# Optimization experiments

Measured on AMD Instinct MI355X. Metric: run time of the kernel, lower is better.

Reference implementation:

```python
import jax, jax.numpy as jnp
import numpy as np


def setup_inputs() -> dict:
    key = jax.random.key(0)
    ks = jax.random.split(key, 6)
    B, S, D = 2, 2048, 1024
    E, DFF = 8, 2048  # E includes always-on expert 0; router sees E-1 routed experts
    scale = 0.02
    return {
        "hidden_states": jax.random.normal(ks[0], (B, S, D), dtype=jnp.float32),
        "router_w": jax.random.normal(ks[1], (D, E - 1), dtype=jnp.float32) * scale,
        "router_b": jnp.zeros((E - 1,), dtype=jnp.float32),
        "wg": jax.random.normal(ks[2], (E, D, DFF), dtype=jnp.float32) * scale,
        "wu": jax.random.normal(ks[3], (E, D, DFF), dtype=jnp.float32) * scale,
        "wd": jax.random.normal(ks[4], (E, DFF, D), dtype=jnp.float32) * scale,
        "top_k": 2,
    }


def _expert_mlp(x, wg_e, wu_e, wd_e):
    # SwiGLU MLP: down( silu(x @ gate) * (x @ up) )
    return (jax.nn.silu(x @ wg_e) * (x @ wu_e)) @ wd_e


def reference(hidden_states, router_w, router_b, wg, wu, wd, top_k):
    B, S, D = hidden_states.shape
    E = wg.shape[0]  # total experts incl. always-on expert 0
    x = hidden_states.reshape(-1, D)  # [T, D]
    T = x.shape[0]

    # Router over E-1 routed experts, softmax in float32
    router_logits = x @ router_w + router_b  # [T, E-1]
    probs = jax.nn.softmax(router_logits.astype(jnp.float32), axis=-1)
    topw, topi = jax.lax.top_k(probs, top_k)  # [T, k]
    topw = topw / jnp.sum(topw, axis=-1, keepdims=True)
    topw = topw.astype(x.dtype)

    # Dense combine weights over routed experts (0 for unselected)
    cw = jnp.zeros((T, E - 1), dtype=x.dtype)
    cw = cw.at[jnp.arange(T)[:, None], topi].add(topw)  # [T, E-1]

    # Always-on expert 0 with weight 1
    out = _expert_mlp(x, wg[0], wu[0], wd[0])  # [T, D]

    # Routed experts 1..E-1 (static small loop over experts)
    for e in range(1, E):
        ye = _expert_mlp(x, wg[e], wu[e], wd[e])  # [T, D]
        out = out + cw[:, e - 1, None] * ye

    return out.reshape(B, S, -1)
```

## Files before the change

### kernel.cpp

```cpp
#include <hip/hip_runtime.h>

#define T_TOK 4096
#define DIM   1024
#define DFF   2048
#define NE    8
#define NR    7
#define MAXNB 71
#define NY    (32 + MAXNB)

typedef __bf16 bf16x8 __attribute__((ext_vector_type(8)));
typedef float  floatx4 __attribute__((ext_vector_type(4)));

__device__ __forceinline__ unsigned short f32_bf16(float f) {
  union { float f; unsigned int u; } v; v.f = f;
  unsigned int u = v.u;
  unsigned int r = (u + 0x7FFFu + ((u >> 16) & 1u)) >> 16;
  return (unsigned short)r;
}

typedef __attribute__((address_space(3))) void lds_void_t;
typedef const __attribute__((address_space(1))) void g_void_t;

__device__ __forceinline__ void gld16(const void* g, void* l) {
  __builtin_amdgcn_global_load_lds((g_void_t*)g, (lds_void_t*)l, 16, 0, 0);
}

__global__ __launch_bounds__(256) void cvt_x_kernel(const float4* __restrict__ in,
                                                    ushort4* __restrict__ out) {
  int i = blockIdx.x * 256 + threadIdx.x;
  float4 v = in[i];
  ushort4 o;
  o.x = f32_bf16(v.x); o.y = f32_bf16(v.y);
  o.z = f32_bf16(v.z); o.w = f32_bf16(v.w);
  out[i] = o;
}

__global__ __launch_bounds__(256) void router_kernel(const float* __restrict__ x,
                                                     const float* __restrict__ rw,
                                                     const float* __restrict__ rb,
                                                     int* __restrict__ idxR,
                                                     float* __restrict__ wslR,
                                                     int* __restrict__ cnt,
                                                     int4* __restrict__ tokE,
                                                     float2* __restrict__ tokW) {
  const int lane = threadIdx.x & 63;
  const int t = blockIdx.x * 4 + (threadIdx.x >> 6);
  const float* xr = x + (size_t)t * DIM;
  float acc[NR];
#pragma unroll
  for (int e = 0; e < NR; e++) acc[e] = 0.f;
  for (int d = lane; d < DIM; d += 64) {
    float xv = xr[d];
#pragma unroll
    for (int e = 0; e < NR; e++) acc[e] += xv * rw[d * NR + e];
  }
#pragma unroll
  for (int off = 32; off > 0; off >>= 1) {
#pragma unroll
    for (int e = 0; e < NR; e++) acc[e] += __shfl_xor(acc[e], off, 64);
  }
  if (lane == 0) {
    float lg[NR];
    float m = -1e30f;
#pragma unroll
    for (int e = 0; e < NR; e++) { lg[e] = acc[e] + rb[e]; m = fmaxf(m, lg[e]); }
    float p[NR], s = 0.f;
#pragma unroll
    for (int e = 0; e < NR; e++) { p[e] = expf(lg[e] - m); s += p[e]; }
#pragma unroll
    for (int e = 0; e < NR; e++) p[e] /= s;
    int i1 = 0;
#pragma unroll
    for (int e = 1; e < NR; e++) if (p[e] > p[i1]) i1 = e;
    int i2 = (i1 == 0) ? 1 : 0;
#pragma unroll
    for (int e = 0; e < NR; e++) if (e != i1 && p[e] > p[i2]) i2 = e;
    float w1 = p[i1], w2 = p[i2], sw = w1 + w2;
    float w1n = w1 / sw, w2n = w2 / sw;
    int s1 = atomicAdd(&cnt[i1], 1);
    idxR[i1 * 4096 + s1] = t; wslR[i1 * 4096 + s1] = w1n;
    int s2 = atomicAdd(&cnt[i2], 1);
    idxR[i2 * 4096 + s2] = t; wslR[i2 * 4096 + s2] = w2n;
    int4 te; te.x = i1; te.y = s1; te.z = i2; te.w = s2;
    tokE[t] = te;
    float2 tw; tw.x = w1n; tw.y = w2n;
    tokW[t] = tw;
  }
}

__global__ __launch_bounds__(256) void sched_kernel(const int* __restrict__ cnt,
                                                    int* __restrict__ idxR,
                                                    float* __restrict__ wslR,
                                                    int4* __restrict__ schedAll,
                                                    int4* __restrict__ schedP,
                                                    int* __restrict__ prefOut,
                                                    int rsb) {
  __shared__ int nb[NR], pref[NR];
  if (threadIdx.x == 0) {
    int p = 0;
    for (int e = 0; e < NR; e++) { int c = cnt[e]; int n = (c + 127) >> 7; nb[e] = n; pref[e] = p; p += n; }
  }
  __syncthreads();
  if (threadIdx.x < NR) prefOut[threadIdx.x] = pref[threadIdx.x];
  for (int e = 0; e < NR; e++) {
    int c = cnt[e], top = nb[e] * 128;
    for (int i = c + (int)threadIdx.x; i < top; i += 256) {
      idxR[e * 4096 + i] = 0; wslR[e * 4096 + i] = 0.f;
    }
  }
  const int NBtot = pref[NR - 1] + nb[NR - 1];
  for (int y = threadIdx.x; y < 32; y += 256) {
    int4 ent; ent.x = 0; ent.y = -1; ent.z = y * 128; ent.w = 0;
    schedAll[y] = ent;
  }
  for (int y = threadIdx.x; y < MAXNB; y += 256) {
    int4 ent; ent.x = -1; ent.y = 0; ent.z = 0; ent.w = 0;
    if (y < NBtot) {
#pragma unroll
      for (int e = 0; e < NR; e++)
        if (y >= pref[e] && y < pref[e] + nb[e]) {
          int rb2 = y - pref[e];
          ent.x = e + 1; ent.y = e * 4096 + rb2 * 128; ent.z = rsb + y * 128;
        }
    }
    schedAll[32 + y] = ent;
  }
  for (int i = threadIdx.x; i < NR * 32; i += 256) {
    int e = i >> 5, rb2 = i & 31;
    int4 ent; ent.w = 0;
    if (rb2 < nb[e]) { ent.x = e + 1; ent.y = e * 4096 + rb2 * 128; ent.z = rb2 * 128; }
    else             { ent.x = -1; ent.y = 0; ent.z = 0; }
    schedP[i] = ent;
  }
}

__global__ __launch_bounds__(256) void transpose_cvt_kernel(
    const float* __restrict__ wg, const float* __restrict__ wu, const float* __restrict__ wd,
    unsigned short* __restrict__ wgt, unsigned short* __restrict__ wut,
    unsigned short* __restrict__ wdt) {
  __shared__ float tile[64][33];
  const int z = blockIdx.z;
  const float* src; unsigned short* dst; int R, C;
  if (z < 8)       { src = wg + (size_t)z * DIM * DFF;        dst = wgt + (size_t)z * DIM * DFF;        R = DIM; C = DFF; }
  else if (z < 16) { src = wu + (size_t)(z - 8) * DIM * DFF;  dst = wut + (size_t)(z - 8) * DIM * DFF;  R = DIM; C = DFF; }
  else             { src = wd + (size_t)(z - 16) * DFF * DIM; dst = wdt + (size_t)(z - 16) * DFF * DIM; R = DFF; C = DIM; }
  const int c0 = blockIdx.x * 32, r0 = blockIdx.y * 64;
  if (c0 >= C || r0 >= R) return;
  const int tx = threadIdx.x & 31, ty = threadIdx.x >> 5;
#pragma unroll
  for (int j = ty; j < 64; j += 8)
    tile[j][tx] = src[(size_t)(r0 + j) * C + c0 + tx];
  __syncthreads();
#pragma unroll
  for (int j = ty; j < 32; j += 8) {
    unsigned int lo = f32_bf16(tile[2 * tx][j]);
    unsigned int hi = f32_bf16(tile[2 * tx + 1][j]);
    *(unsigned int*)(dst + (size_t)(c0 + j) * R + r0 + 2 * tx) = lo | (hi << 16);
  }
}

__global__ __launch_bounds__(512, 2) void gemm1_kernel(
    const unsigned short* __restrict__ xb, const unsigned short* __restrict__ wgt,
    const unsigned short* __restrict__ wut, const int* __restrict__ idxR,
    const int4* __restrict__ sched, unsigned short* __restrict__ h, int gx) {
  const int nblk = gridDim.x;
  int bid = blockIdx.x;
  { int q = nblk >> 3, r = nblk & 7, xc = bid & 7, p = bid >> 3;
    bid = (xc < r ? xc * (q + 1) : r * (q + 1) + (xc - r) * q) + p; }
  const int by = bid / gx, bx = bid - by * gx;
  const int4 ent = sched[by];
  if (ent.x < 0) return;
  __shared__ unsigned short smem[3 * 24576];
  const int tid = threadIdx.x, lane = tid & 63, wid = tid >> 6;
  const int n0 = bx * 128;
  const int wm64 = (wid >> 2) * 64, wn32 = (wid & 3) * 32;
  const int fr = lane & 15, kq8 = lane >> 4, x7 = fr & 7;
  const int r0 = tid >> 3;
  const int c8 = ((tid & 7) ^ (r0 & 7)) * 8;
  int tok0, tok1;
  if (ent.y < 0) { tok0 = ent.z + r0; tok1 = ent.z + r0 + 64; }
  else           { tok0 = idxR[ent.y + r0]; tok1 = idxR[ent.y + r0 + 64]; }
  const unsigned short* wgt_e = wgt + (size_t)ent.x * DIM * DFF;
  const unsigned short* wut_e = wut + (size_t)ent.x * DIM * DFF;
  const unsigned short* gA0 = xb + (size_t)tok0 * DIM + c8;
  const unsigned short* gA1 = xb + (size_t)tok1 * DIM + c8;
  const unsigned short* gG0 = wgt_e + (size_t)(n0 + r0) * DIM + c8;
  const unsigned short* gG1 = gG0 + (size_t)64 * DIM;
  const unsigned short* gU0 = wut_e + (size_t)(n0 + r0) * DIM + c8;
  const unsigned short* gU1 = gU0 + (size_t)64 * DIM;
  int offA[2][2], offB[2][2];
#pragma unroll
  for (int mi = 0; mi < 2; mi++)
#pragma unroll
    for (int kk = 0; kk < 2; kk++)
      offA[mi][kk] = (wm64 + mi * 16 + fr) * 64 + (((kk * 4 + kq8) ^ x7) * 8);
#pragma unroll
  for (int ni = 0; ni < 2; ni++)
#pragma unroll
    for (int kk = 0; kk < 2; kk++)
      offB[ni][kk] = (wn32 + ni * 16 + fr) * 64 + (((kk * 4 + kq8) ^ x7) * 8);
  floatx4 accg[4][2], accu[4][2];
  const floatx4 z4 = {0.f, 0.f, 0.f, 0.f};
#pragma unroll
  for (int i = 0; i < 4; i++)
#pragma unroll
    for (int j = 0; j < 2; j++) { accg[i][j] = z4; accu[i][j] = z4; }
  {
    unsigned short* d = smem + tid * 8;
    gld16(gA0, d);             gld16(gA1, d + 4096);
    gld16(gG0, d + 8192);      gld16(gG1, d + 12288);
    gld16(gU0, d + 16384);     gld16(gU1, d + 20480);
    unsigned short* e = smem + 24576 + tid * 8;
    gld16(gA0 + 64, e);        gld16(gA1 + 64, e + 4096);
    gld16(gG0 + 64, e + 8192); gld16(gG1 + 64, e + 12288);
    gld16(gU0 + 64, e + 16384); gld16(gU1 + 64, e + 20480);
  }
  asm volatile("s_waitcnt vmcnt(6)" ::: "memory");
  __builtin_amdgcn_s_barrier();
  int b = 0;
  for (int k = 0; k < 16; ++k) {
    const unsigned short* Bb = smem + b * 24576;
    int b2 = b + 2; if (b2 >= 3) b2 -= 3;
    unsigned short* db2 = smem + b2 * 24576 + tid * 8;
    const bool pf = (k < 14);
    const int kt = (k + 2) * 64;
    bf16x8 a[2][2], bg[2][2], bu[2][2];
#pragma unroll
    for (int mi = 0; mi < 2; mi++)
#pragma unroll
      for (int kk = 0; kk < 2; kk++) a[mi][kk] = *(const bf16x8*)(Bb + offA[mi][kk]);
#pragma unroll
    for (int ni = 0; ni < 2; ni++)
#pragma unroll
      for (int kk = 0; kk < 2; kk++) bg[ni][kk] = *(const bf16x8*)(Bb + 8192 + offB[ni][kk]);
    if (pf) { gld16(gA0 + kt, db2); gld16(gA1 + kt, db2 + 4096); }
    __builtin_amdgcn_sched_barrier(0);
    __builtin_amdgcn_s_barrier();
    __builtin_amdgcn_s_setprio(1);
#pragma unroll
    for (int mi = 0; mi < 2; mi++)
#pragma unroll
      for (int ni = 0; ni < 2; ni++)
#pragma unroll
        for (int kk = 0; kk < 2; kk++)
          accg[mi][ni] = __builtin_amdgcn_mfma_f32_16x16x32_bf16(a[mi][kk], bg[ni][kk], accg[mi][ni], 0, 0, 0);
    __builtin_amdgcn_s_setprio(0);
    __builtin_amdgcn_sched_barrier(0);
    __builtin_amdgcn_s_barrier();
#pragma unroll
    for (int ni = 0; ni < 2; ni++)
#pragma unroll
      for (int kk = 0; kk < 2; kk++) bu[ni][kk] = *(const bf16x8*)(Bb + 16384 + offB[ni][kk]);
    if (pf) { gld16(gG0 + kt, db2 + 8192); gld16(gG1 + kt, db2 + 12288); }
    __builtin_amdgcn_sched_barrier(0);
    __builtin_amdgcn_s_barrier();
    __builtin_amdgcn_s_setprio(1);
#pragma unroll
    for (int mi = 0; mi < 2; mi++)
#pragma unroll
      for (int ni = 0; ni < 2; ni++)
#pragma unroll
        for (int kk = 0; kk < 2; kk++)
          accu[mi][ni] = __builtin_amdgcn_mfma_f32_16x16x32_bf16(a[mi][kk], bu[ni][kk], accu[mi][ni], 0, 0, 0);
    __builtin_amdgcn_s_setprio(0);
    __builtin_amdgcn_sched_barrier(0);
    __builtin_amdgcn_s_barrier();
#pragma unroll
    for (int mi = 0; mi < 2; mi++)
#pragma unroll
      for (int kk = 0; kk < 2; kk++) a[mi][kk] = *(const bf16x8*)(Bb + 2048 + offA[mi][kk]);
    if (pf) { gld16(gU0 + kt, db2 + 16384); gld16(gU1 + kt, db2 + 20480); }
    __builtin_amdgcn_sched_barrier(0);
    __builtin_amdgcn_s_barrier();
    __builtin_amdgcn_s_setprio(1);
#pragma unroll
    for (int mi = 0; mi < 2; mi++)
#pragma unroll
      for (int ni = 0; ni < 2; ni++)
#pragma unroll
        for (int kk = 0; kk < 2; kk++) {
          accg[2 + mi][ni] = __builtin_amdgcn_mfma_f32_16x16x32_bf16(a[mi][kk], bg[ni][kk], accg[2 + mi][ni], 0, 0, 0);
          accu[2 + mi][ni] = __builtin_amdgcn_mfma_f32_16x16x32_bf16(a[mi][kk], bu[ni][kk], accu[2 + mi][ni], 0, 0, 0);
        }
    __builtin_amdgcn_s_setprio(0);
    __builtin_amdgcn_sched_barrier(0);
    if (k < 14)       asm volatile("s_waitcnt vmcnt(6)" ::: "memory");
    else if (k == 14) asm volatile("s_waitcnt vmcnt(0)" ::: "memory");
    __builtin_amdgcn_s_barrier();
    b++; if (b == 3) b = 0;
  }
  const int rb = kq8 * 4;
#pragma unroll
  for (int mi = 0; mi < 4; mi++)
#pragma unroll
    for (int ni = 0; ni < 2; ni++)
#pragma unroll
      for (int r = 0; r < 4; r++) {
        int row = ent.z + wm64 + mi * 16 + rb + r;
        int col = n0 + wn32 + ni * 16 + fr;
        float g = accg[mi][ni][r], u = accu[mi][ni][r];
        float hv = (g / (1.f + __expf(-g))) * u;
        h[(size_t)row * DFF + col] = f32_bf16(hv);
      }
}

__global__ __launch_bounds__(512, 2) void gemm2_kernel(
    const unsigned short* __restrict__ hsrc, const unsigned short* __restrict__ wdt,
    const int4* __restrict__ sched, float* __restrict__ y, int gx) {
  const int nblk = gridDim.x;
  int bid = blockIdx.x;
  { int q = nblk >> 3, r = nblk & 7, xc = bid & 7, p = bid >> 3;
    bid = (xc < r ? xc * (q + 1) : r * (q + 1) + (xc - r) * q) + p; }
  const int by = bid / gx, bx = bid - by * gx;
  const int4 ent = sched[by];
  if (ent.x < 0) return;
  __shared__ unsigned short smem[3 * 24576];
  const int tid = threadIdx.x, lane = tid & 63, wid = tid >> 6;
  const int n0 = bx * 256;
  const int wm64 = (wid >> 2) * 64, wn64 = (wid & 3) * 64;
  const int fr = lane & 15, kq8 = lane >> 4, x7 = fr & 7;
  const int r0 = tid >> 3;
  const int c8 = ((tid & 7) ^ (r0 & 7)) * 8;
  const unsigned short* wdt_e = wdt + (size_t)ent.x * DFF * DIM;
  const unsigned short* gA0 = hsrc + (size_t)(ent.z + r0) * DFF + c8;
  const unsigned short* gA1 = gA0 + (size_t)64 * DFF;
  const unsigned short* gB0 = wdt_e + (size_t)(n0 + r0) * DFF + c8;
  const unsigned short* gB1 = gB0 + (size_t)64 * DFF;
  const unsigned short* gB2 = gB0 + (size_t)128 * DFF;
  const unsigned short* gB3 = gB0 + (size_t)192 * DFF;
  int offA[2][2], offB[2][2];
#pragma unroll
  for (int mi = 0; mi < 2; mi++)
#pragma unroll
    for (int kk = 0; kk < 2; kk++)
      offA[mi][kk] = (wm64 + mi * 16 + fr) * 64 + (((kk * 4 + kq8) ^ x7) * 8);
#pragma unroll
  for (int ni = 0; ni < 2; ni++)
#pragma unroll
    for (int kk = 0; kk < 2; kk++)
      offB[ni][kk] = (wn64 + ni * 16 + fr) * 64 + (((kk * 4 + kq8) ^ x7) * 8);
  floatx4 acc[4][4];
  const floatx4 z4 = {0.f, 0.f, 0.f, 0.f};
#pragma unroll
  for (int i = 0; i < 4; i++)
#pragma unroll
    for (int j = 0; j < 4; j++) acc[i][j] = z4;
  {
    unsigned short* d = smem + tid * 8;
    gld16(gA0, d);             gld16(gA1, d + 4096);
    gld16(gB0, d + 8192);      gld16(gB1, d + 12288);
    gld16(gB2, d + 16384);     gld16(gB3, d + 20480);
    unsigned short* e = smem + 24576 + tid * 8;
    gld16(gA0 + 64, e);        gld16(gA1 + 64, e + 4096);
    gld16(gB0 + 64, e + 8192); gld16(gB1 + 64, e + 12288);
    gld16(gB2 + 64, e + 16384); gld16(gB3 + 64, e + 20480);
  }
  asm volatile("s_waitcnt vmcnt(6)" ::: "memory");
  __builtin_amdgcn_s_barrier();
  int b = 0;
  for (int k = 0; k < 32; ++k) {
    const unsigned short* Bb = smem + b * 24576;
    int b2 = b + 2; if (b2 >= 3) b2 -= 3;
    unsigned short* db2 = smem + b2 * 24576 + tid * 8;
    const bool pf = (k < 30);
    const int kt = (k + 2) * 64;
    bf16x8 a[2][2], b0[2][2], b1[2][2];
#pragma unroll
    for (int mi = 0; mi < 2; mi++)
#pragma unroll
      for (int kk = 0; kk < 2; kk++) a[mi][kk] = *(const bf16x8*)(Bb + offA[mi][kk]);
#pragma unroll
    for (int ni = 0; ni < 2; ni++)
#pragma unroll
      for (int kk = 0; kk < 2; kk++) b0[ni][kk] = *(const bf16x8*)(Bb + 8192 + offB[ni][kk]);
    if (pf) { gld16(gA0 + kt, db2); gld16(gA1 + kt, db2 + 4096); }
    __builtin_amdgcn_sched_barrier(0);
    __builtin_amdgcn_s_barrier();
    __builtin_amdgcn_s_setprio(1);
#pragma unroll
    for (int mi = 0; mi < 2; mi++)
#pragma unroll
      for (int ni = 0; ni < 2; ni++)
#pragma unroll
        for (int kk = 0; kk < 2; kk++)
          acc[mi][ni] = __builtin_amdgcn_mfma_f32_16x16x32_bf16(a[mi][kk], b0[ni][kk], acc[mi][ni], 0, 0, 0);
    __builtin_amdgcn_s_setprio(0);
    __builtin_amdgcn_sched_barrier(0);
    __builtin_amdgcn_s_barrier();
#pragma unroll
    for (int ni = 0; ni < 2; ni++)
#pragma unroll
      for (int kk = 0; kk < 2; kk++) b1[ni][kk] = *(const bf16x8*)(Bb + 10240 + offB[ni][kk]);
    if (pf) { gld16(gB0 + kt, db2 + 8192); gld16(gB1 + kt, db2 + 12288); }
    __builtin_amdgcn_sched_barrier(0);
    __builtin_amdgcn_s_barrier();
    __builtin_amdgcn_s_setprio(1);
#pragma unroll
    for (int mi = 0; mi < 2; mi++)
#pragma unroll
      for (int ni = 0; ni < 2; ni++)
#pragma unroll
        for (int kk = 0; kk < 2; kk++)
          acc[mi][2 + ni] = __builtin_amdgcn_mfma_f32_16x16x32_bf16(a[mi][kk], b1[ni][kk], acc[mi][2 + ni], 0, 0, 0);
    __builtin_amdgcn_s_setprio(0);
    __builtin_amdgcn_sched_barrier(0);
    __builtin_amdgcn_s_barrier();
#pragma unroll
    for (int mi = 0; mi < 2; mi++)
#pragma unroll
      for (int kk = 0; kk < 2; kk++) a[mi][kk] = *(const bf16x8*)(Bb + 2048 + offA[mi][kk]);
    if (pf) { gld16(gB2 + kt, db2 + 16384); gld16(gB3 + kt, db2 + 20480); }
    __builtin_amdgcn_sched_barrier(0);
    __builtin_amdgcn_s_barrier();
    __builtin_amdgcn_s_setprio(1);
#pragma unroll
    for (int mi = 0; mi < 2; mi++)
#pragma unroll
      for (int ni = 0; ni < 2; ni++)
#pragma unroll
        for (int kk = 0; kk < 2; kk++) {
          acc[2 + mi][ni]     = __builtin_amdgcn_mfma_f32_16x16x32_bf16(a[mi][kk], b0[ni][kk], acc[2 + mi][ni], 0, 0, 0);
          acc[2 + mi][2 + ni] = __builtin_amdgcn_mfma_f32_16x16x32_bf16(a[mi][kk], b1[ni][kk], acc[2 + mi][2 + ni], 0, 0, 0);
        }
    __builtin_amdgcn_s_setprio(0);
    __builtin_amdgcn_sched_barrier(0);
    if (k < 30)       asm volatile("s_waitcnt vmcnt(6)" ::: "memory");
    else if (k == 30) asm volatile("s_waitcnt vmcnt(0)" ::: "memory");
    __builtin_amdgcn_s_barrier();
    b++; if (b == 3) b = 0;
  }
  const int rb = kq8 * 4;
#pragma unroll
  for (int mi = 0; mi < 4; mi++)
#pragma unroll
    for (int ni = 0; ni < 4; ni++)
#pragma unroll
      for (int r = 0; r < 4; r++)
        y[(size_t)(ent.z + wm64 + mi * 16 + rb + r) * DIM + n0 + wn64 + ni * 16 + fr] = acc[mi][ni][r];
}

__global__ __launch_bounds__(256) void gemm2_atomic_kernel(
    const unsigned short* __restrict__ h, const unsigned short* __restrict__ wdt,
    const int* __restrict__ idxR, const float* __restrict__ wslR,
    const int4* __restrict__ sched, float* __restrict__ out) {
  const int4 ent = sched[blockIdx.y];
  if (ent.x < 0) return;
  __shared__ unsigned short As[128 * 32];
  __shared__ unsigned short Bs[128 * 32];
  const int tid = threadIdx.x, lane = tid & 63, wid = tid >> 6;
  const int n0 = blockIdx.x * 128;
  const int wm = (wid >> 1) * 64, wn = (wid & 1) * 64;
  floatx4 acc[4][4];
  const floatx4 z4 = {0.f, 0.f, 0.f, 0.f};
#pragma unroll
  for (int i = 0; i < 4; i++)
#pragma unroll
    for (int j = 0; j < 4; j++) acc[i][j] = z4;
  const unsigned short* wdt_e = wdt + (size_t)ent.x * DFF * DIM;
  const int srow = tid >> 2, scol = (tid & 3) * 8;
  const unsigned short* ap0 = h + (size_t)(ent.z + srow) * DFF + scol;
  const unsigned short* ap1 = ap0 + (size_t)64 * DFF;
  const unsigned short* bp0 = wdt_e + (size_t)(n0 + srow) * DFF + scol;
  const unsigned short* bp1 = bp0 + (size_t)64 * DFF;
  unsigned short* as0 = As + tid * 8;
  unsigned short* as1 = As + (256 + tid) * 8;
  unsigned short* bs0 = Bs + tid * 8;
  unsigned short* bs1 = Bs + (256 + tid) * 8;
  const int fr = lane & 15, kq = (lane >> 4) * 8;
  for (int k0 = 0; k0 < DFF; k0 += 32) {
    __syncthreads();
    gld16(ap0 + k0, as0); gld16(ap1 + k0, as1);
    gld16(bp0 + k0, bs0); gld16(bp1 + k0, bs1);
    __syncthreads();
    bf16x8 af[4], bf[4];
#pragma unroll
    for (int mi = 0; mi < 4; mi++) af[mi] = *(const bf16x8*)(As + (wm + mi * 16 + fr) * 32 + kq);
#pragma unroll
    for (int ni = 0; ni < 4; ni++) bf[ni] = *(const bf16x8*)(Bs + (wn + ni * 16 + fr) * 32 + kq);
#pragma unroll
    for (int mi = 0; mi < 4; mi++)
#pragma unroll
      for (int ni = 0; ni < 4; ni++)
        acc[mi][ni] = __builtin_amdgcn_mfma_f32_16x16x32_bf16(af[mi], bf[ni], acc[mi][ni], 0, 0, 0);
  }
  const int rb0 = wm + (lane >> 4) * 4;
  const int cb0 = n0 + wn + fr;
#pragma unroll
  for (int mi = 0; mi < 4; mi++)
#pragma unroll
    for (int r = 0; r < 4; r++) {
      int lrow = rb0 + mi * 16 + r;
      if (ent.y < 0) {
        int tok = ent.z + lrow;
#pragma unroll
        for (int ni = 0; ni < 4; ni++)
          out[(size_t)tok * DIM + cb0 + ni * 16] = acc[mi][ni][r];
      } else {
        int tok = idxR[ent.y + lrow];
        float s = wslR[ent.y + lrow];
        if (s != 0.f) {
#pragma unroll
          for (int ni = 0; ni < 4; ni++)
            atomicAdd(&out[(size_t)tok * DIM + cb0 + ni * 16], s * acc[mi][ni][r]);
        }
      }
    }
}

__global__ __launch_bounds__(256) void combine_kernel(const float* __restrict__ y,
                                                      const int4* __restrict__ tokE,
                                                      const float2* __restrict__ tokW,
                                                      const int* __restrict__ pref,
                                                      float* __restrict__ out) {
  const int t = blockIdx.x;
  const int c = threadIdx.x * 4;
  int4 te = tokE[t];
  float2 tw = tokW[t];
  int p1 = 4096 + pref[te.x] * 128 + te.y;
  int p2 = 4096 + pref[te.z] * 128 + te.w;
  float4 a = *(const float4*)(y + (size_t)t * DIM + c);
  float4 b = *(const float4*)(y + (size_t)p1 * DIM + c);
  float4 d = *(const float4*)(y + (size_t)p2 * DIM + c);
  float4 o;
  o.x = a.x + tw.x * b.x + tw.y * d.x;
  o.y = a.y + tw.x * b.y + tw.y * d.y;
  o.z = a.z + tw.x * b.z + tw.y * d.z;
  o.w = a.w + tw.x * b.w + tw.y * d.w;
  *(float4*)(out + (size_t)t * DIM + c) = o;
}

extern "C" void kernel_launch(void* const* d_in, const int* in_sizes, int n_in,
                              void* d_out, int out_size, void* d_ws, size_t ws_size,
                              hipStream_t stream) {
  const float* x  = (const float*)d_in[0];
  const float* rw = (const float*)d_in[1];
  const float* rb = (const float*)d_in[2];
  const float* wg = (const float*)d_in[3];
  const float* wu = (const float*)d_in[4];
  const float* wd = (const float*)d_in[5];
  float* out = (float*)d_out;

  const bool modeA = ws_size >= (size_t)163300000;
  const bool modeB = !modeA && ws_size >= (size_t)146700000;
  const size_t H_ROWS = modeA ? 13184 : (modeB ? 9088 : 4096);
  const int rsb = modeA ? 4096 : 0;

  char* p = (char*)d_ws;
  unsigned short* xb  = (unsigned short*)p; p += (size_t)T_TOK * DIM * 2;
  unsigned short* h   = (unsigned short*)p; p += H_ROWS * DFF * 2;
  unsigned short* wgt = (unsigned short*)p;
  float*          y   = (float*)p;          p += (size_t)NE * DIM * DFF * 2;
  unsigned short* wut = (unsigned short*)p; p += (size_t)NE * DIM * DFF * 2;
  unsigned short* wdt = (unsigned short*)p; p += (size_t)NE * DIM * DFF * 2;
  int*   idxR = (int*)p;   p += (size_t)NR * 4096 * 4;
  float* wslR;
  if (modeA) { wslR = (float*)wdt; }
  else       { wslR = (float*)p; p += (size_t)NR * 4096 * 4; }
  int*   cnt  = (int*)p;      p += 64;
  int*   pref = (int*)p;      p += 64;
  int4*  schedAll = (int4*)p; p += 2048;
  int4*  schedP   = (int4*)p; p += 4096;
  int4*  tokE = (int4*)p;     p += (size_t)T_TOK * 16;
  float2* tokW = (float2*)p;  p += (size_t)T_TOK * 8;

  cvt_x_kernel<<<dim3(T_TOK * DIM / 4 / 256), 256, 0, stream>>>((const float4*)x, (ushort4*)xb);
  hipMemsetAsync(cnt, 0, 64, stream);
  router_kernel<<<dim3(T_TOK / 4), 256, 0, stream>>>(x, rw, rb, idxR, wslR, cnt, tokE, tokW);
  sched_kernel<<<dim3(1), 256, 0, stream>>>(cnt, idxR, wslR, schedAll, schedP, pref, rsb);
  transpose_cvt_kernel<<<dim3(64, 32, 24), 256, 0, stream>>>(wg, wu, wd, wgt, wut, wdt);

  if (modeA) {
    gemm1_kernel<<<dim3((DFF / 128) * NY), 512, 0, stream>>>(xb, wgt, wut, idxR, schedAll, h, DFF / 128);
    gemm2_kernel<<<dim3((DIM / 256) * NY), 512, 0, stream>>>(h, wdt, schedAll, y, DIM / 256);
    combine_kernel<<<dim3(T_TOK), 256, 0, stream>>>(y, tokE, tokW, pref, out);
  } else if (modeB) {
    gemm1_kernel<<<dim3((DFF / 128) * 32), 512, 0, stream>>>(xb, wgt, wut, idxR, schedAll, h, DFF / 128);
    gemm2_atomic_kernel<<<dim3(DIM / 128, 32), 256, 0, stream>>>(h, wdt, idxR, wslR, schedAll, out);
    gemm1_kernel<<<dim3((DFF / 128) * MAXNB), 512, 0, stream>>>(xb, wgt, wut, idxR, schedAll + 32, h, DFF / 128);
    gemm2_atomic_kernel<<<dim3(DIM / 128, MAXNB), 256, 0, stream>>>(h, wdt, idxR, wslR, schedAll + 32, out);
  } else {
    gemm1_kernel<<<dim3((DFF / 128) * 32), 512, 0, stream>>>(xb, wgt, wut, idxR, schedAll, h, DFF / 128);
    gemm2_atomic_kernel<<<dim3(DIM / 128, 32), 256, 0, stream>>>(h, wdt, idxR, wslR, schedAll, out);
    for (int e = 0; e < NR; e++) {
      gemm1_kernel<<<dim3((DFF / 128) * 32), 512, 0, stream>>>(xb, wgt, wut, idxR, schedP + e * 32, h, DFF / 128);
      gemm2_atomic_kernel<<<dim3(DIM / 128, 32), 256, 0, stream>>>(h, wdt, idxR, wslR, schedP + e * 32, out);
    }
  }
}
```

Baseline: 566.9 us.

## Collapse GEMM K-loop into single-phase prefetch and change block-to-tile mapping

The GEMM1 and GEMM2 main loops drop the three-phase split, which had interleaved LDS reads, partial global prefetches and several s_barriers per K step. Each step now issues all six async global-to-LDS prefetches up front, reads all A and B fragments at once, and runs all MFMAs in one block. Separately, GEMM1's block index decode now makes the row-block (expert/token group) the fast-varying index, so consecutive blocks share weight columns. This is meant to cut barrier overhead and improve L2 reuse of weights, at the cost of more live VGPRs (larger fragment arrays) and less fine-grained overlap.

```diff
diff --git a/kernel.cpp b/kernel.cpp
--- a/kernel.cpp
+++ b/kernel.cpp
@@ -162,12 +162,12 @@
 __global__ __launch_bounds__(512, 2) void gemm1_kernel(
     const unsigned short* __restrict__ xb, const unsigned short* __restrict__ wgt,
     const unsigned short* __restrict__ wut, const int* __restrict__ idxR,
-    const int4* __restrict__ sched, unsigned short* __restrict__ h, int gx) {
+    const int4* __restrict__ sched, unsigned short* __restrict__ h, int gy) {
   const int nblk = gridDim.x;
   int bid = blockIdx.x;
   { int q = nblk >> 3, r = nblk & 7, xc = bid & 7, p = bid >> 3;
     bid = (xc < r ? xc * (q + 1) : r * (q + 1) + (xc - r) * q) + p; }
-  const int by = bid / gx, bx = bid - by * gx;
+  const int bx = bid / gy, by = bid - bx * gy;
   const int4 ent = sched[by];
   if (ent.x < 0) return;
   __shared__ unsigned short smem[3 * 24576];
@@ -188,9 +188,9 @@
   const unsigned short* gG1 = gG0 + (size_t)64 * DIM;
   const unsigned short* gU0 = wut_e + (size_t)(n0 + r0) * DIM + c8;
   const unsigned short* gU1 = gU0 + (size_t)64 * DIM;
-  int offA[2][2], offB[2][2];
-#pragma unroll
-  for (int mi = 0; mi < 2; mi++)
+  int offA[4][2], offB[2][2];
+#pragma unroll
+  for (int mi = 0; mi < 4; mi++)
 #pragma unroll
     for (int kk = 0; kk < 2; kk++)
       offA[mi][kk] = (wm64 + mi * 16 + fr) * 64 + (((kk * 4 + kq8) ^ x7) * 8);
@@ -222,66 +222,40 @@
     const unsigned short* Bb = smem + b * 24576;
     int b2 = b + 2; if (b2 >= 3) b2 -= 3;
     unsigned short* db2 = smem + b2 * 24576 + tid * 8;
-    const bool pf = (k < 14);
-    const int kt = (k + 2) * 64;
-    bf16x8 a[2][2], bg[2][2], bu[2][2];
-#pragma unroll
-    for (int mi = 0; mi < 2; mi++)
+    if (k < 14) {
+      const int kt = (k + 2) * 64;
+      gld16(gA0 + kt, db2);         gld16(gA1 + kt, db2 + 4096);
+      gld16(gG0 + kt, db2 + 8192);  gld16(gG1 + kt, db2 + 12288);
+      gld16(gU0 + kt, db2 + 16384); gld16(gU1 + kt, db2 + 20480);
+    }
+    __builtin_amdgcn_sched_barrier(0);
+    bf16x8 a[4][2], bg[2][2], bu[2][2];
+#pragma unroll
+    for (int mi = 0; mi < 4; mi++)
 #pragma unroll
       for (int kk = 0; kk < 2; kk++) a[mi][kk] = *(const bf16x8*)(Bb + offA[mi][kk]);
 #pragma unroll
     for (int ni = 0; ni < 2; ni++)
 #pragma unroll
-      for (int kk = 0; kk < 2; kk++) bg[ni][kk] = *(const bf16x8*)(Bb + 8192 + offB[ni][kk]);
-    if (pf) { gld16(gA0 + kt, db2); gld16(gA1 + kt, db2 + 4096); }
-    __builtin_amdgcn_sched_barrier(0);
-    __builtin_amdgcn_s_barrier();
+      for (int kk = 0; kk < 2; kk++) {
+        bg[ni][kk] = *(const bf16x8*)(Bb + 8192 + offB[ni][kk]);
+        bu[ni][kk] = *(const bf16x8*)(Bb + 16384 + offB[ni][kk]);
+      }
     __builtin_amdgcn_s_setprio(1);
 #pragma unroll
-    for (int mi = 0; mi < 2; mi++)
+    for (int mi = 0; mi < 4; mi++)
 #pragma unroll
       for (int ni = 0; ni < 2; ni++)
 #pragma unroll
         for (int kk = 0; kk < 2; kk++)
           accg[mi][ni] = __builtin_amdgcn_mfma_f32_16x16x32_bf16(a[mi][kk], bg[ni][kk], accg[mi][ni], 0, 0, 0);
-    __builtin_amdgcn_s_setprio(0);
-    __builtin_amdgcn_sched_barrier(0);
-    __builtin_amdgcn_s_barrier();
-#pragma unroll
-    for (int ni = 0; ni < 2; ni++)
-#pragma unroll
-      for (int kk = 0; kk < 2; kk++) bu[ni][kk] = *(const bf16x8*)(Bb + 16384 + offB[ni][kk]);
-    if (pf) { gld16(gG0 + kt, db2 + 8192); gld16(gG1 + kt, db2 + 12288); }
-    __builtin_amdgcn_sched_barrier(0);
-    __builtin_amdgcn_s_barrier();
-    __builtin_amdgcn_s_setprio(1);
-#pragma unroll
-    for (int mi = 0; mi < 2; mi++)
+#pragma unroll
+    for (int mi = 0; mi < 4; mi++)
 #pragma unroll
       for (int ni = 0; ni < 2; ni++)
 #pragma unroll
         for (int kk = 0; kk < 2; kk++)
           accu[mi][ni] = __builtin_amdgcn_mfma_f32_16x16x32_bf16(a[mi][kk], bu[ni][kk], accu[mi][ni], 0, 0, 0);
-    __builtin_amdgcn_s_setprio(0);
-    __builtin_amdgcn_sched_barrier(0);
-    __builtin_amdgcn_s_barrier();
-#pragma unroll
-    for (int mi = 0; mi < 2; mi++)
-#pragma unroll
-      for (int kk = 0; kk < 2; kk++) a[mi][kk] = *(const bf16x8*)(Bb + 2048 + offA[mi][kk]);
-    if (pf) { gld16(gU0 + kt, db2 + 16384); gld16(gU1 + kt, db2 + 20480); }
-    __builtin_amdgcn_sched_barrier(0);
-    __builtin_amdgcn_s_barrier();
-    __builtin_amdgcn_s_setprio(1);
-#pragma unroll
-    for (int mi = 0; mi < 2; mi++)
-#pragma unroll
-      for (int ni = 0; ni < 2; ni++)
-#pragma unroll
-        for (int kk = 0; kk < 2; kk++) {
-          accg[2 + mi][ni] = __builtin_amdgcn_mfma_f32_16x16x32_bf16(a[mi][kk], bg[ni][kk], accg[2 + mi][ni], 0, 0, 0);
-          accu[2 + mi][ni] = __builtin_amdgcn_mfma_f32_16x16x32_bf16(a[mi][kk], bu[ni][kk], accu[2 + mi][ni], 0, 0, 0);
-        }
     __builtin_amdgcn_s_setprio(0);
     __builtin_amdgcn_sched_barrier(0);
     if (k < 14)       asm volatile("s_waitcnt vmcnt(6)" ::: "memory");
@@ -328,9 +302,9 @@
   const unsigned short* gB1 = gB0 + (size_t)64 * DFF;
   const unsigned short* gB2 = gB0 + (size_t)128 * DFF;
   const unsigned short* gB3 = gB0 + (size_t)192 * DFF;
-  int offA[2][2], offB[2][2];
-#pragma unroll
-  for (int mi = 0; mi < 2; mi++)
+  int offA[4][2], offB[2][2];
+#pragma unroll
+  for (int mi = 0; mi < 4; mi++)
 #pragma unroll
     for (int kk = 0; kk < 2; kk++)
       offA[mi][kk] = (wm64 + mi * 16 + fr) * 64 + (((kk * 4 + kq8) ^ x7) * 8);
@@ -362,65 +336,34 @@
     const unsigned short* Bb = smem + b * 24576;
     int b2 = b + 2; if (b2 >= 3) b2 -= 3;
     unsigned short* db2 = smem + b2 * 24576 + tid * 8;
-    const bool pf = (k < 30);
-    const int kt = (k + 2) * 64;
-    bf16x8 a[2][2], b0[2][2], b1[2][2];
-#pragma unroll
-    for (int mi = 0; mi < 2; mi++)
+    if (k < 30) {
+      const int kt = (k + 2) * 64;
+      gld16(gA0 + kt, db2);         gld16(gA1 + kt, db2 + 4096);
+      gld16(gB0 + kt, db2 + 8192);  gld16(gB1 + kt, db2 + 12288);
+      gld16(gB2 + kt, db2 + 16384); gld16(gB3 + kt, db2 + 20480);
+    }
+    __builtin_amdgcn_sched_barrier(0);
+    bf16x8 a[4][2], b0[2][2], b1[2][2];
+#pragma unroll
+    for (int mi = 0; mi < 4; mi++)
 #pragma unroll
       for (int kk = 0; kk < 2; kk++) a[mi][kk] = *(const bf16x8*)(Bb + offA[mi][kk]);
 #pragma unroll
     for (int ni = 0; ni < 2; ni++)
 #pragma unroll
-      for (int kk = 0; kk < 2; kk++) b0[ni][kk] = *(const bf16x8*)(Bb + 8192 + offB[ni][kk]);
-    if (pf) { gld16(gA0 + kt, db2); gld16(gA1 + kt, db2 + 4096); }
-    __builtin_amdgcn_sched_barrier(0);
-    __builtin_amdgcn_s_barrier();
+      for (int kk = 0; kk < 2; kk++) {
+        b0[ni][kk] = *(const bf16x8*)(Bb + 8192 + offB[ni][kk]);
+        b1[ni][kk] = *(const bf16x8*)(Bb + 10240 + offB[ni][kk]);
+      }
     __builtin_amdgcn_s_setprio(1);
 #pragma unroll
-    for (int mi = 0; mi < 2; mi++)
+    for (int mi = 0; mi < 4; mi++)
 #pragma unroll
       for (int ni = 0; ni < 2; ni++)
 #pragma unroll
-        for (int kk = 0; kk < 2; kk++)
-          acc[mi][ni] = __builtin_amdgcn_mfma_f32_16x16x32_bf16(a[mi][kk], b0[ni][kk], acc[mi][ni], 0, 0, 0);
-    __builtin_amdgcn_s_setprio(0);
-    __builtin_amdgcn_sched_barrier(0);
-    __builtin_amdgcn_s_barrier();
-#pragma unroll
-    for (int ni = 0; ni < 2; ni++)
-#pragma unroll
-      for (int kk = 0; kk < 2; kk++) b1[ni][kk] = *(const bf16x8*)(Bb + 10240 + offB[ni][kk]);
-    if (pf) { gld16(gB0 + kt, db2 + 8192); gld16(gB1 + kt, db2 + 12288); }
-    __builtin_amdgcn_sched_barrier(0);
-    __builtin_amdgcn_s_barrier();
-    __builtin_amdgcn_s_setprio(1);
-#pragma unroll
-    for (int mi = 0; mi < 2; mi++)
-#pragma unroll
-      for (int ni = 0; ni < 2; ni++)
-#pragma unroll
-        for (int kk = 0; kk < 2; kk++)
+        for (int kk = 0; kk < 2; kk++) {
+          acc[mi][ni]     = __builtin_amdgcn_mfma_f32_16x16x32_bf16(a[mi][kk], b0[ni][kk], acc[mi][ni], 0, 0, 0);
           acc[mi][2 + ni] = __builtin_amdgcn_mfma_f32_16x16x32_bf16(a[mi][kk], b1[ni][kk], acc[mi][2 + ni], 0, 0, 0);
-    __builtin_amdgcn_s_setprio(0);
-    __builtin_amdgcn_sched_barrier(0);
-    __builtin_amdgcn_s_barrier();
-#pragma unroll
-    for (int mi = 0; mi < 2; mi++)
-#pragma unroll
-      for (int kk = 0; kk < 2; kk++) a[mi][kk] = *(const bf16x8*)(Bb + 2048 + offA[mi][kk]);
-    if (pf) { gld16(gB2 + kt, db2 + 16384); gld16(gB3 + kt, db2 + 20480); }
-    __builtin_amdgcn_sched_barrier(0);
-    __builtin_amdgcn_s_barrier();
-    __builtin_amdgcn_s_setprio(1);
-#pragma unroll
-    for (int mi = 0; mi < 2; mi++)
-#pragma unroll
-      for (int ni = 0; ni < 2; ni++)
-#pragma unroll
-        for (int kk = 0; kk < 2; kk++) {
-          acc[2 + mi][ni]     = __builtin_amdgcn_mfma_f32_16x16x32_bf16(a[mi][kk], b0[ni][kk], acc[2 + mi][ni], 0, 0, 0);
-          acc[2 + mi][2 + ni] = __builtin_amdgcn_mfma_f32_16x16x32_bf16(a[mi][kk], b1[ni][kk], acc[2 + mi][2 + ni], 0, 0, 0);
         }
     __builtin_amdgcn_s_setprio(0);
     __builtin_amdgcn_sched_barrier(0);
@@ -570,19 +513,19 @@
   transpose_cvt_kernel<<<dim3(64, 32, 24), 256, 0, stream>>>(wg, wu, wd, wgt, wut, wdt);
 
   if (modeA) {
-    gemm1_kernel<<<dim3((DFF / 128) * NY), 512, 0, stream>>>(xb, wgt, wut, idxR, schedAll, h, DFF / 128);
+    gemm1_kernel<<<dim3((DFF / 128) * NY), 512, 0, stream>>>(xb, wgt, wut, idxR, schedAll, h, NY);
     gemm2_kernel<<<dim3((DIM / 256) * NY), 512, 0, stream>>>(h, wdt, schedAll, y, DIM / 256);
     combine_kernel<<<dim3(T_TOK), 256, 0, stream>>>(y, tokE, tokW, pref, out);
   } else if (modeB) {
-    gemm1_kernel<<<dim3((DFF / 128) * 32), 512, 0, stream>>>(xb, wgt, wut, idxR, schedAll, h, DFF / 128);
+    gemm1_kernel<<<dim3((DFF / 128) * 32), 512, 0, stream>>>(xb, wgt, wut, idxR, schedAll, h, 32);
     gemm2_atomic_kernel<<<dim3(DIM / 128, 32), 256, 0, stream>>>(h, wdt, idxR, wslR, schedAll, out);
-    gemm1_kernel<<<dim3((DFF / 128) * MAXNB), 512, 0, stream>>>(xb, wgt, wut, idxR, schedAll + 32, h, DFF / 128);
+    gemm1_kernel<<<dim3((DFF / 128) * MAXNB), 512, 0, stream>>>(xb, wgt, wut, idxR, schedAll + 32, h, MAXNB);
     gemm2_atomic_kernel<<<dim3(DIM / 128, MAXNB), 256, 0, stream>>>(h, wdt, idxR, wslR, schedAll + 32, out);
   } else {
-    gemm1_kernel<<<dim3((DFF / 128) * 32), 512, 0, stream>>>(xb, wgt, wut, idxR, schedAll, h, DFF / 128);
+    gemm1_kernel<<<dim3((DFF / 128) * 32), 512, 0, stream>>>(xb, wgt, wut, idxR, schedAll, h, 32);
     gemm2_atomic_kernel<<<dim3(DIM / 128, 32), 256, 0, stream>>>(h, wdt, idxR, wslR, schedAll, out);
     for (int e = 0; e < NR; e++) {
-      gemm1_kernel<<<dim3((DFF / 128) * 32), 512, 0, stream>>>(xb, wgt, wut, idxR, schedP + e * 32, h, DFF / 128);
+      gemm1_kernel<<<dim3((DFF / 128) * 32), 512, 0, stream>>>(xb, wgt, wut, idxR, schedP + e * 32, h, 32);
       gemm2_atomic_kernel<<<dim3(DIM / 128, 32), 256, 0, stream>>>(h, wdt, idxR, wslR, schedP + e * 32, out);
     }
   }
```

Measured after the change: 546.8 us. -3.5%, faster.
